# Optimization experiments

Measured on AMD Instinct MI355X. Metric: run time of the kernel, lower is better.

## Reference

```python
import jax, jax.numpy as jnp
import numpy as np

B, S, D, H = 2, 2048, 1024, 16
DH = D // H  # dim_per_head = 64


def setup_inputs() -> dict:
    key = jax.random.key(0)
    ks = jax.random.split(key, 12)
    scale = 1.0 / np.sqrt(D)
    inp = {
        "key": jax.random.normal(ks[0], (B, S, D), jnp.float32),
        "value": jax.random.normal(ks[1], (B, S, D), jnp.float32),
        "query": jax.random.normal(ks[2], (B, S, D), jnp.float32),
        "mask": jnp.zeros((B, S, S), dtype=bool),
        # nn.Linear weights stored as [out, in]; we keep [in, out] for x @ W
        "Wk": jax.random.normal(ks[3], (D, D), jnp.float32) * scale,
        "bk": jnp.zeros((D,), jnp.float32),
        "Wv": jax.random.normal(ks[4], (D, D), jnp.float32) * scale,
        "bv": jnp.zeros((D,), jnp.float32),
        "Wq": jax.random.normal(ks[5], (D, D), jnp.float32) * scale,
        "bq": jnp.zeros((D,), jnp.float32),
        "Wo": jax.random.normal(ks[6], (D, D), jnp.float32) * scale,
        "bo": jnp.zeros((D,), jnp.float32),
    }
    return inp


def reference(key, value, query, mask, Wk, bk, Wv, bv, Wq, bq, Wo, bo):
    # project and split heads: [B, S, D] -> [B, H, S, DH]
    def shape(x):
        return x.reshape(B, S, H, DH).transpose(0, 2, 1, 3)

    k = shape(key @ Wk + bk)
    v = shape(value @ Wv + bv)
    q = shape(query @ Wq + bq) / jnp.sqrt(jnp.asarray(DH, key.dtype))

    # scores: [B, H, Sq, Sk]
    scores = jnp.einsum("bhqd,bhkd->bhqk", q, k)
    scores = jnp.where(mask[:, None, :, :], jnp.asarray(-1e10, scores.dtype), scores)
    attn = jax.nn.softmax(scores, axis=-1)
    # dropout is identity in eval mode
    context = jnp.einsum("bhqk,bhkd->bhqd", attn, v)
    context = context.transpose(0, 2, 1, 3).reshape(B, S, D)
    output = context @ Wo + bo
    return output, attn
```

## Files before the change

### kernel.cpp

```cpp
#include <hip/hip_runtime.h>

#define B_  2
#define S_  2048
#define D_  1024
#define H_  16

typedef _Float16 h8 __attribute__((ext_vector_type(8)));
typedef _Float16 h4 __attribute__((ext_vector_type(4)));
typedef float f4 __attribute__((ext_vector_type(4)));

static __device__ __forceinline__ f4 mfma16(h8 a, h8 b, f4 c) {
  return __builtin_amdgcn_mfma_f32_16x16x32_f16(a, b, c, 0, 0, 0);
}

static __device__ __forceinline__ void gload16(const void* g, void* l) {
  __builtin_amdgcn_global_load_lds(
      (const __attribute__((address_space(1))) void*)g,
      (__attribute__((address_space(3))) void*)l, 16, 0, 0);
}

struct C3 { const float* in[3]; _Float16* out[3]; };
__global__ __launch_bounds__(256) void cvt3_kernel(C3 c) {
  const float* in = c.in[blockIdx.y];
  _Float16* out = c.out[blockIdx.y];
  const size_t i = ((size_t)blockIdx.x * 256 + threadIdx.x) * 8;
  float4 a = *(const float4*)(in + i);
  float4 b = *(const float4*)(in + i + 4);
  h8 v;
  v[0]=(_Float16)a.x; v[1]=(_Float16)a.y; v[2]=(_Float16)a.z; v[3]=(_Float16)a.w;
  v[4]=(_Float16)b.x; v[5]=(_Float16)b.y; v[6]=(_Float16)b.z; v[7]=(_Float16)b.w;
  *(h8*)(out + i) = v;
}

struct W4 { const float* w[4]; _Float16* wt[4]; };
__global__ __launch_bounds__(256) void wtrans4_kernel(W4 a) {
  const float* W = a.w[blockIdx.z];
  _Float16* WT = a.wt[blockIdx.z];
  __shared__ float tile[64][65];
  const int t = threadIdx.x;
  const int bi = blockIdx.x * 64;
  const int bj = blockIdx.y * 64;
  const int row = t >> 2, c0 = (t & 3) * 16;
  const float* src = W + (size_t)(bi + row) * D_ + bj + c0;
#pragma unroll
  for (int j = 0; j < 4; j++) {
    float4 v = *(const float4*)(src + j * 4);
    tile[row][c0 + j*4 + 0] = v.x; tile[row][c0 + j*4 + 1] = v.y;
    tile[row][c0 + j*4 + 2] = v.z; tile[row][c0 + j*4 + 3] = v.w;
  }
  __syncthreads();
  h8 o0, o1;
#pragma unroll
  for (int j = 0; j < 8; j++) o0[j] = (_Float16)tile[c0 + j][row];
#pragma unroll
  for (int j = 0; j < 8; j++) o1[j] = (_Float16)tile[c0 + 8 + j][row];
  _Float16* dst = WT + (size_t)(bj + row) * D_ + bi + c0;
  *(h8*)(dst)     = o0;
  *(h8*)(dst + 8) = o1;
}

__global__ __launch_bounds__(256) void maskflag_kernel(const unsigned char* __restrict__ mask,
                                                       unsigned char* __restrict__ flags) {
  __shared__ int s;
  const int t = threadIdx.x;
  const int kt = blockIdx.x, qb = blockIdx.y, b = blockIdx.z;
  if (t == 0) s = 0;
  __syncthreads();
  const unsigned char* mp = mask + ((size_t)(b * S_ + qb * 128 + (t >> 1))) * S_
                          + kt * 64 + (t & 1) * 32;
  const uint4* p = (const uint4*)mp;
  uint4 v = p[0], w = p[1];
  unsigned int o = v.x | v.y | v.z | v.w | w.x | w.y | w.z | w.w;
  if (o) s = 1;
  __syncthreads();
  if (t == 0) flags[((size_t)b * 16 + qb) * 32 + kt] = (unsigned char)s;
}

struct GArg { const _Float16* A; const _Float16* BT; const float* bias;
              void* out; float scale; int mode; };
struct G3 { GArg a[3]; };

__global__ __launch_bounds__(512, 4) void gemmz_kernel(G3 G) {
  const GArg g = G.a[blockIdx.z];
  const _Float16* __restrict__ A  = g.A;
  const _Float16* __restrict__ BT = g.BT;
  __shared__ _Float16 Ash[128 * 64];
  __shared__ _Float16 Bsh[128 * 64];
  const int t = threadIdx.x, lane = t & 63, wave = t >> 6;
  const int lrow = lane & 15, lq = lane >> 4;
  const int m0 = blockIdx.x * 128, n0 = blockIdx.y * 128;
  const int wm = wave >> 2, wn = wave & 3;
  f4 acc[4][2];
#pragma unroll
  for (int i = 0; i < 4; i++)
#pragma unroll
    for (int j = 0; j < 2; j++) acc[i][j] = f4{0.f, 0.f, 0.f, 0.f};
  float bb[2];
#pragma unroll
  for (int j = 0; j < 2; j++) bb[j] = g.bias[n0 + wn*32 + j*16 + lrow];

  const int srow = t >> 3;
  const int lch  = (t & 7) ^ (srow & 7);
  const _Float16* a0 = A  + (size_t)(m0 + srow)      * D_ + lch * 8;
  const _Float16* a1 = A  + (size_t)(m0 + 64 + srow) * D_ + lch * 8;
  const _Float16* b0 = BT + (size_t)(n0 + srow)      * D_ + lch * 8;
  const _Float16* b1 = BT + (size_t)(n0 + 64 + srow) * D_ + lch * 8;
  char* adst0 = (char*)Ash + wave * 1024;
  char* adst1 = (char*)Ash + 8192 + wave * 1024;
  char* bdst0 = (char*)Bsh + wave * 1024;
  char* bdst1 = (char*)Bsh + 8192 + wave * 1024;

  for (int k0 = 0; k0 < D_; k0 += 64) {
    gload16(a0 + k0, adst0);
    gload16(a1 + k0, adst1);
    gload16(b0 + k0, bdst0);
    gload16(b1 + k0, bdst1);
    __syncthreads();
#pragma unroll
    for (int kf = 0; kf < 2; kf++) {
      h8 af[4], bf[2];
#pragma unroll
      for (int i = 0; i < 4; i++) {
        int rr = wm*64 + i*16 + lrow;
        int ch = (kf*4 + lq) ^ (rr & 7);
        af[i] = *(h8*)((char*)Ash + rr*128 + ch*16);
      }
#pragma unroll
      for (int j = 0; j < 2; j++) {
        int rr = wn*32 + j*16 + lrow;
        int ch = (kf*4 + lq) ^ (rr & 7);
        bf[j] = *(h8*)((char*)Bsh + rr*128 + ch*16);
      }
#pragma unroll
      for (int i = 0; i < 4; i++)
#pragma unroll
        for (int j = 0; j < 2; j++)
          acc[i][j] = mfma16(af[i], bf[j], acc[i][j]);
    }
    __syncthreads();
  }

  if (g.mode == 0) {
    _Float16* out = (_Float16*)g.out;
#pragma unroll
    for (int i = 0; i < 4; i++) {
      int m = m0 + wm*64 + i*16 + lq*4;
#pragma unroll
      for (int j = 0; j < 2; j++) {
        int n = n0 + wn*32 + j*16 + lrow;
#pragma unroll
        for (int r = 0; r < 4; r++)
          out[(size_t)(m + r) * D_ + n] = (_Float16)((acc[i][j][r] + bb[j]) * g.scale);
      }
    }
  } else if (g.mode == 1) {
    _Float16* out = (_Float16*)g.out;
#pragma unroll
    for (int i = 0; i < 4; i++) {
      int m = m0 + wm*64 + i*16 + lq*4;
      int b = m >> 11, s = m & (S_ - 1);
#pragma unroll
      for (int j = 0; j < 2; j++) {
        int n = n0 + wn*32 + j*16 + lrow;
        int hh = n >> 6, dh = n & 63;
        h4 hv;
#pragma unroll
        for (int r = 0; r < 4; r++) hv[r] = (_Float16)(acc[i][j][r] + bb[j]);
        *(h4*)(out + ((size_t)((b * H_ + hh) * 64 + dh)) * S_ + s) = hv;
      }
    }
  } else {
    float* out = (float*)g.out;
#pragma unroll
    for (int i = 0; i < 4; i++) {
      int m = m0 + wm*64 + i*16 + lq*4;
#pragma unroll
      for (int j = 0; j < 2; j++) {
        int n = n0 + wn*32 + j*16 + lrow;
#pragma unroll
        for (int r = 0; r < 4; r++)
          out[(size_t)(m + r) * D_ + n] = acc[i][j][r] + bb[j];
      }
    }
  }
}


__global__ __launch_bounds__(256, 4) void attnA_kernel(
    const _Float16* __restrict__ Qp, const _Float16* __restrict__ Kp,
    const unsigned char* __restrict__ mask, const unsigned char* __restrict__ flags,
    float* __restrict__ Lbuf)
{
  __shared__ _Float16 Kt[256 * 64];
  const int t = threadIdx.x, lane = t & 63, wave = t >> 6;
  const int lrow = lane & 15, lq = lane >> 4;
  const int logical = ((blockIdx.x & 7) << 7) + (blockIdx.x >> 3);
  const int bh = logical >> 5, qb = logical & 31;
  const int b = bh >> 4, h = bh & 15;
  const int q0 = qb * 64, qw = q0 + wave * 16;

  h8 qf0, qf1;
  {
    const _Float16* qp = Qp + ((size_t)(b * S_ + qw + lrow)) * D_ + h * 64 + lq * 8;
    qf0 = *(const h8*)qp;
    qf1 = *(const h8*)(qp + 32);
  }

  const int srow = t >> 3, klch = (t & 7) ^ (srow & 7);
  const _Float16* ksrc = Kp + ((size_t)(b * S_ + srow)) * D_ + h * 64 + klch * 8;
  char* kdst = (char*)Kt + wave * 1024;
  const unsigned char* mflags = flags + ((size_t)(b * 16 + (qb >> 1))) * 32;

  float lsum[4] = {0.f, 0.f, 0.f, 0.f};
  for (int kt = 0; kt < S_; kt += 256) {
#pragma unroll
    for (int rnd = 0; rnd < 8; rnd++)
      gload16(ksrc + (size_t)(kt + rnd * 32) * D_, kdst + rnd * 4096);
    __syncthreads();
    const unsigned char* mrow = mask + ((size_t)(b * S_ + qw + lq*4)) * S_ + kt + lrow;
#pragma unroll
    for (int c = 0; c < 16; c++) {
      int kr = c*16 + lrow, sx = kr & 7;
      h8 k0 = *(h8*)((char*)Kt + kr*128 + ((lq     ^ sx) << 4));
      h8 k1 = *(h8*)((char*)Kt + kr*128 + (((4+lq) ^ sx) << 4));
      f4 a = f4{0.f, 0.f, 0.f, 0.f};
      a = mfma16(qf0, k0, a);
      a = mfma16(qf1, k1, a);
      if (mflags[(kt >> 6) + (c >> 2)]) {
#pragma unroll
        for (int r = 0; r < 4; r++)
          if (mrow[(size_t)r * S_ + c*16]) a[r] = -1e10f;
      }
#pragma unroll
      for (int r = 0; r < 4; r++) lsum[r] += __expf(fminf(a[r], 75.f));
    }
    __syncthreads();
  }

#pragma unroll
  for (int r = 0; r < 4; r++) {
    float cs = lsum[r];
#pragma unroll
    for (int d = 1; d < 16; d <<= 1) cs += __shfl_xor(cs, d);
    if (lrow == 0) Lbuf[((size_t)bh << 11) + qw + lq*4 + r] = 1.0f / cs;
  }
}

__global__ __launch_bounds__(256, 4) void attnB_kernel(
    const _Float16* __restrict__ Qp, const _Float16* __restrict__ Kp,
    const _Float16* __restrict__ VpT, const unsigned char* __restrict__ mask,
    const unsigned char* __restrict__ flags, const float* __restrict__ Lbuf,
    float* __restrict__ attn, _Float16* __restrict__ CtxH)
{
  __shared__ _Float16 Kt[128 * 64];
  __shared__ _Float16 Vt[64 * 128];
  __shared__ _Float16 Pt[64 * 64];
  const int t = threadIdx.x, lane = t & 63, wave = t >> 6;
  const int lrow = lane & 15, lq = lane >> 4;
  const int logical = ((blockIdx.x & 7) << 7) + (blockIdx.x >> 3);
  const int bh = logical >> 5, qb = logical & 31;
  const int b = bh >> 4, h = bh & 15;
  const int q0 = qb * 64, qw = q0 + wave * 16;

  h8 qf0, qf1;
  {
    const _Float16* qp = Qp + ((size_t)(b * S_ + qw + lrow)) * D_ + h * 64 + lq * 8;
    qf0 = *(const h8*)qp;
    qf1 = *(const h8*)(qp + 32);
  }
  float li[4];
#pragma unroll
  for (int r = 0; r < 4; r++) li[r] = Lbuf[((size_t)bh << 11) + qw + lq*4 + r];

  const int srow = t >> 3, klch = (t & 7) ^ (srow & 7);
  const _Float16* ksrc = Kp + ((size_t)(b * S_ + srow)) * D_ + h * 64 + klch * 8;
  char* kdst = (char*)Kt + wave * 1024;
  const int vrow = t >> 4, vlch = (t & 15) ^ (vrow & 15);
  const _Float16* vsrc = VpT + (size_t)bh * 64 * S_ + (size_t)vrow * S_ + vlch * 8;
  char* vdst = (char*)Vt + wave * 1024;
  const unsigned char* mflags = flags + ((size_t)(b * 16 + (qb >> 1))) * 32;

  f4 ctx[4];
#pragma unroll
  for (int dt = 0; dt < 4; dt++) ctx[dt] = f4{0.f, 0.f, 0.f, 0.f};

  for (int kt = 0; kt < S_; kt += 128) {
#pragma unroll
    for (int rnd = 0; rnd < 4; rnd++)
      gload16(ksrc + (size_t)(kt + rnd * 32) * D_, kdst + rnd * 4096);
#pragma unroll
    for (int rnd = 0; rnd < 4; rnd++)
      gload16(vsrc + (size_t)(rnd * 16) * S_ + kt, vdst + rnd * 4096);
    __syncthreads();

#pragma unroll
    for (int hh = 0; hh < 2; hh++) {
      const int kbase = kt + hh * 64;
      const bool mf = mflags[kbase >> 6] != 0;
      const unsigned char* mrow = mask + ((size_t)(b * S_ + qw + lq*4)) * S_ + kbase + lrow;
      const int prw = wave*16 + lq*4;
#pragma unroll
      for (int c = 0; c < 4; c++) {
        int kr = hh*64 + c*16 + lrow, sx = kr & 7;
        h8 k0 = *(h8*)((char*)Kt + kr*128 + ((lq     ^ sx) << 4));
        h8 k1 = *(h8*)((char*)Kt + kr*128 + (((4+lq) ^ sx) << 4));
        f4 a = f4{0.f, 0.f, 0.f, 0.f};
        a = mfma16(qf0, k0, a);
        a = mfma16(qf1, k1, a);
        if (mf) {
#pragma unroll
          for (int r = 0; r < 4; r++)
            if (mrow[(size_t)r * S_ + c*16]) a[r] = -1e10f;
        }
        float* ap = attn + ((size_t)bh * S_ + qw + lq*4) * S_ + kbase + c*16 + lrow;
        int eb = c*32 + lrow*2;
#pragma unroll
        for (int r = 0; r < 4; r++) {
          float p = __expf(fminf(a[r], 75.f)) * li[r];
          ap[(size_t)r * S_] = p;
          int rw = prw + r;
          *(_Float16*)((char*)Pt + rw*128 + ((((eb >> 4) ^ (rw & 7))) << 4) + (eb & 15))
              = (_Float16)p;
        }
      }
      {
        int pr2 = wave*16 + lrow, sxp = pr2 & 7;
        h8 pf0 = *(h8*)((char*)Pt + pr2*128 + (((    lq) ^ sxp) << 4));
        h8 pf1 = *(h8*)((char*)Pt + pr2*128 + (((4 + lq) ^ sxp) << 4));
#pragma unroll
        for (int dt = 0; dt < 4; dt++) {
          int vr = dt*16 + lrow, sxv = vr & 15;
          h8 vf0 = *(h8*)((char*)Vt + vr*256 + (((hh*8     + lq) ^ sxv) << 4));
          h8 vf1 = *(h8*)((char*)Vt + vr*256 + (((hh*8 + 4 + lq) ^ sxv) << 4));
          ctx[dt] = mfma16(pf0, vf0, ctx[dt]);
          ctx[dt] = mfma16(pf1, vf1, ctx[dt]);
        }
      }
    }
    __syncthreads();
  }

  _Float16* cp = CtxH + ((size_t)(b * S_ + qw + lq*4)) * D_ + h * 64 + lrow;
#pragma unroll
  for (int dt = 0; dt < 4; dt++)
#pragma unroll
    for (int r = 0; r < 4; r++)
      cp[(size_t)r * D_ + dt*16] = (_Float16)ctx[dt][r];
}

extern "C" void kernel_launch(void* const* d_in, const int* in_sizes, int n_in,
                              void* d_out, int out_size, void* d_ws, size_t ws_size,
                              hipStream_t stream) {
  const float* key   = (const float*)d_in[0];
  const float* value = (const float*)d_in[1];
  const float* query = (const float*)d_in[2];
  const unsigned char* mask = (const unsigned char*)d_in[3];
  const float* Wk = (const float*)d_in[4];
  const float* bk = (const float*)d_in[5];
  const float* Wv = (const float*)d_in[6];
  const float* bv = (const float*)d_in[7];
  const float* Wq = (const float*)d_in[8];
  const float* bq = (const float*)d_in[9];
  const float* Wo = (const float*)d_in[10];
  const float* bo = (const float*)d_in[11];

  char* ws = (char*)d_ws;
  _Float16* WkT  = (_Float16*)(ws + 0);
  _Float16* WvT  = (_Float16*)(ws + (size_t)2  * 1024 * 1024);
  _Float16* WqT  = (_Float16*)(ws + (size_t)4  * 1024 * 1024);
  _Float16* WoT  = (_Float16*)(ws + (size_t)6  * 1024 * 1024);
  _Float16* Qp   = (_Float16*)(ws + (size_t)8  * 1024 * 1024);
  _Float16* Kp   = (_Float16*)(ws + (size_t)16 * 1024 * 1024);
  _Float16* VpT  = (_Float16*)(ws + (size_t)24 * 1024 * 1024);
  _Float16* CtxH = (_Float16*)(ws + (size_t)32 * 1024 * 1024);
  unsigned char* flags = (unsigned char*)(ws + (size_t)40 * 1024 * 1024);
  float* Lbuf = (float*)(ws + (size_t)40 * 1024 * 1024 + 64 * 1024);

  float* outp = (float*)d_out;
  float* attn = outp + (size_t)B_ * S_ * D_;
  _Float16* qH = (_Float16*)(attn);
  _Float16* kH = (_Float16*)((char*)attn + (size_t)8  * 1024 * 1024);
  _Float16* vH = (_Float16*)((char*)attn + (size_t)16 * 1024 * 1024);

  C3 c{{query, key, value}, {qH, kH, vH}};
  cvt3_kernel<<<dim3(2048, 3), 256, 0, stream>>>(c);

  W4 w{{Wk, Wv, Wq, Wo}, {WkT, WvT, WqT, WoT}};
  wtrans4_kernel<<<dim3(16, 16, 4), 256, 0, stream>>>(w);

  maskflag_kernel<<<dim3(32, 16, 2), 256, 0, stream>>>(mask, flags);

  G3 gp{{{qH, WqT, bq, Qp, 0.125f, 0},
         {kH, WkT, bk, Kp, 1.0f,   0},
         {vH, WvT, bv, VpT, 1.0f,  1}}};
  gemmz_kernel<<<dim3(32, 8, 3), 512, 0, stream>>>(gp);

  attnA_kernel<<<1024, 256, 0, stream>>>(Qp, Kp, mask, flags, Lbuf);
  attnB_kernel<<<1024, 256, 0, stream>>>(Qp, Kp, VpT, mask, flags, Lbuf, attn, CtxH);

  G3 go{{{CtxH, WoT, bo, outp, 1.0f, 2},
         {nullptr, nullptr, nullptr, nullptr, 0.f, 2},
         {nullptr, nullptr, nullptr, nullptr, 0.f, 2}}};
  gemmz_kernel<<<dim3(32, 8, 1), 512, 0, stream>>>(go);
}
```

Measured before the change: 304.2 us.

## Double-buffer K/V tiles and process 128 query rows per attention block

Both attention kernels now give each wave 32 query rows instead of 16, so every K/V fragment read from shared memory feeds two MFMA groups. The grid is halved to 512 blocks. K and V tiles are double-buffered, so the next tile's global-to-LDS load is issued before the current tile is computed, which removes one barrier per iteration. The cost is twice the LDS and more registers, with occupancy hints cut from 4 to 2 blocks per CU.

Result: slower. 310.6 us (+2.1%).

```diff
diff --git a/kernel.cpp b/kernel.cpp
--- a/kernel.cpp
+++ b/kernel.cpp
@@ -186,166 +186,226 @@
 }
 
 
-__global__ __launch_bounds__(256, 4) void attnA_kernel(
+__global__ __launch_bounds__(256, 2) void attnA_kernel(
     const _Float16* __restrict__ Qp, const _Float16* __restrict__ Kp,
     const unsigned char* __restrict__ mask, const unsigned char* __restrict__ flags,
     float* __restrict__ Lbuf)
 {
-  __shared__ _Float16 Kt[256 * 64];
+  __shared__ _Float16 Kt[2 * 256 * 64];
   const int t = threadIdx.x, lane = t & 63, wave = t >> 6;
   const int lrow = lane & 15, lq = lane >> 4;
-  const int logical = ((blockIdx.x & 7) << 7) + (blockIdx.x >> 3);
-  const int bh = logical >> 5, qb = logical & 31;
+  const int logical = ((blockIdx.x & 7) << 6) + (blockIdx.x >> 3);
+  const int bh = logical >> 4, qb = logical & 15;
   const int b = bh >> 4, h = bh & 15;
-  const int q0 = qb * 64, qw = q0 + wave * 16;
-
-  h8 qf0, qf1;
-  {
-    const _Float16* qp = Qp + ((size_t)(b * S_ + qw + lrow)) * D_ + h * 64 + lq * 8;
-    qf0 = *(const h8*)qp;
-    qf1 = *(const h8*)(qp + 32);
+  const int q0 = qb * 128, qw = q0 + wave * 32;
+
+  h8 qf0[2], qf1[2];
+#pragma unroll
+  for (int g = 0; g < 2; g++) {
+    const _Float16* qp = Qp + ((size_t)(b * S_ + qw + g*16 + lrow)) * D_ + h * 64 + lq * 8;
+    qf0[g] = *(const h8*)qp;
+    qf1[g] = *(const h8*)(qp + 32);
   }
 
   const int srow = t >> 3, klch = (t & 7) ^ (srow & 7);
   const _Float16* ksrc = Kp + ((size_t)(b * S_ + srow)) * D_ + h * 64 + klch * 8;
-  char* kdst = (char*)Kt + wave * 1024;
-  const unsigned char* mflags = flags + ((size_t)(b * 16 + (qb >> 1))) * 32;
-
-  float lsum[4] = {0.f, 0.f, 0.f, 0.f};
+  const unsigned char* mflags = flags + ((size_t)(b * 16 + qb)) * 32;
+  const unsigned char* mrow0 = mask + ((size_t)(b * S_ + qw + lq*4)) * S_ + lrow;
+
+  float lsum[2][4];
+#pragma unroll
+  for (int g = 0; g < 2; g++)
+#pragma unroll
+    for (int r = 0; r < 4; r++) lsum[g][r] = 0.f;
+
+  {
+    char* kd = (char*)Kt + wave * 1024;
+#pragma unroll
+    for (int rnd = 0; rnd < 8; rnd++)
+      gload16(ksrc + (size_t)(rnd * 32) * D_, kd + rnd * 4096);
+  }
+  __syncthreads();
+  int cur = 0;
+
   for (int kt = 0; kt < S_; kt += 256) {
-#pragma unroll
-    for (int rnd = 0; rnd < 8; rnd++)
-      gload16(ksrc + (size_t)(kt + rnd * 32) * D_, kdst + rnd * 4096);
-    __syncthreads();
-    const unsigned char* mrow = mask + ((size_t)(b * S_ + qw + lq*4)) * S_ + kt + lrow;
+    if (kt + 256 < S_) {
+      char* kd = (char*)Kt + (cur ^ 1) * 32768 + wave * 1024;
+#pragma unroll
+      for (int rnd = 0; rnd < 8; rnd++)
+        gload16(ksrc + (size_t)(kt + 256 + rnd * 32) * D_, kd + rnd * 4096);
+    }
+    char* kb = (char*)Kt + cur * 32768;
 #pragma unroll
     for (int c = 0; c < 16; c++) {
       int kr = c*16 + lrow, sx = kr & 7;
-      h8 k0 = *(h8*)((char*)Kt + kr*128 + ((lq     ^ sx) << 4));
-      h8 k1 = *(h8*)((char*)Kt + kr*128 + (((4+lq) ^ sx) << 4));
-      f4 a = f4{0.f, 0.f, 0.f, 0.f};
-      a = mfma16(qf0, k0, a);
-      a = mfma16(qf1, k1, a);
-      if (mflags[(kt >> 6) + (c >> 2)]) {
-#pragma unroll
-        for (int r = 0; r < 4; r++)
-          if (mrow[(size_t)r * S_ + c*16]) a[r] = -1e10f;
-      }
-#pragma unroll
-      for (int r = 0; r < 4; r++) lsum[r] += __expf(fminf(a[r], 75.f));
+      h8 k0 = *(h8*)(kb + kr*128 + ((lq     ^ sx) << 4));
+      h8 k1 = *(h8*)(kb + kr*128 + (((4+lq) ^ sx) << 4));
+      const bool mf = mflags[(kt >> 6) + (c >> 2)] != 0;
+#pragma unroll
+      for (int g = 0; g < 2; g++) {
+        f4 a = f4{0.f, 0.f, 0.f, 0.f};
+        a = mfma16(qf0[g], k0, a);
+        a = mfma16(qf1[g], k1, a);
+        if (mf) {
+          const unsigned char* mr = mrow0 + (size_t)(g*16) * S_ + kt + c*16;
+#pragma unroll
+          for (int r = 0; r < 4; r++)
+            if (mr[(size_t)r * S_]) a[r] = -1e10f;
+        }
+#pragma unroll
+        for (int r = 0; r < 4; r++) lsum[g][r] += __expf(fminf(a[r], 75.f));
+      }
     }
     __syncthreads();
-  }
-
-#pragma unroll
-  for (int r = 0; r < 4; r++) {
-    float cs = lsum[r];
-#pragma unroll
-    for (int d = 1; d < 16; d <<= 1) cs += __shfl_xor(cs, d);
-    if (lrow == 0) Lbuf[((size_t)bh << 11) + qw + lq*4 + r] = 1.0f / cs;
-  }
-}
-
-__global__ __launch_bounds__(256, 4) void attnB_kernel(
+    cur ^= 1;
+  }
+
+#pragma unroll
+  for (int g = 0; g < 2; g++)
+#pragma unroll
+    for (int r = 0; r < 4; r++) {
+      float cs = lsum[g][r];
+#pragma unroll
+      for (int d = 1; d < 16; d <<= 1) cs += __shfl_xor(cs, d);
+      if (lrow == 0) Lbuf[((size_t)bh << 11) + qw + g*16 + lq*4 + r] = 1.0f / cs;
+    }
+}
+
+__global__ __launch_bounds__(256, 2) void attnB_kernel(
     const _Float16* __restrict__ Qp, const _Float16* __restrict__ Kp,
     const _Float16* __restrict__ VpT, const unsigned char* __restrict__ mask,
     const unsigned char* __restrict__ flags, const float* __restrict__ Lbuf,
     float* __restrict__ attn, _Float16* __restrict__ CtxH)
 {
-  __shared__ _Float16 Kt[128 * 64];
-  __shared__ _Float16 Vt[64 * 128];
-  __shared__ _Float16 Pt[64 * 64];
+  __shared__ _Float16 Kt[2 * 128 * 64];
+  __shared__ _Float16 Vt[2 * 64 * 128];
+  __shared__ _Float16 Pt[128 * 64];
   const int t = threadIdx.x, lane = t & 63, wave = t >> 6;
   const int lrow = lane & 15, lq = lane >> 4;
-  const int logical = ((blockIdx.x & 7) << 7) + (blockIdx.x >> 3);
-  const int bh = logical >> 5, qb = logical & 31;
+  const int logical = ((blockIdx.x & 7) << 6) + (blockIdx.x >> 3);
+  const int bh = logical >> 4, qb = logical & 15;
   const int b = bh >> 4, h = bh & 15;
-  const int q0 = qb * 64, qw = q0 + wave * 16;
-
-  h8 qf0, qf1;
-  {
-    const _Float16* qp = Qp + ((size_t)(b * S_ + qw + lrow)) * D_ + h * 64 + lq * 8;
-    qf0 = *(const h8*)qp;
-    qf1 = *(const h8*)(qp + 32);
-  }
-  float li[4];
-#pragma unroll
-  for (int r = 0; r < 4; r++) li[r] = Lbuf[((size_t)bh << 11) + qw + lq*4 + r];
+  const int q0 = qb * 128, qw = q0 + wave * 32;
+
+  h8 qf0[2], qf1[2];
+  float li[2][4];
+#pragma unroll
+  for (int g = 0; g < 2; g++) {
+    const _Float16* qp = Qp + ((size_t)(b * S_ + qw + g*16 + lrow)) * D_ + h * 64 + lq * 8;
+    qf0[g] = *(const h8*)qp;
+    qf1[g] = *(const h8*)(qp + 32);
+#pragma unroll
+    for (int r = 0; r < 4; r++)
+      li[g][r] = Lbuf[((size_t)bh << 11) + qw + g*16 + lq*4 + r];
+  }
 
   const int srow = t >> 3, klch = (t & 7) ^ (srow & 7);
   const _Float16* ksrc = Kp + ((size_t)(b * S_ + srow)) * D_ + h * 64 + klch * 8;
-  char* kdst = (char*)Kt + wave * 1024;
   const int vrow = t >> 4, vlch = (t & 15) ^ (vrow & 15);
   const _Float16* vsrc = VpT + (size_t)bh * 64 * S_ + (size_t)vrow * S_ + vlch * 8;
-  char* vdst = (char*)Vt + wave * 1024;
-  const unsigned char* mflags = flags + ((size_t)(b * 16 + (qb >> 1))) * 32;
-
-  f4 ctx[4];
-#pragma unroll
-  for (int dt = 0; dt < 4; dt++) ctx[dt] = f4{0.f, 0.f, 0.f, 0.f};
+  const unsigned char* mflags = flags + ((size_t)(b * 16 + qb)) * 32;
+  const unsigned char* mrow0 = mask + ((size_t)(b * S_ + qw + lq*4)) * S_ + lrow;
+
+  f4 ctx[2][4];
+#pragma unroll
+  for (int g = 0; g < 2; g++)
+#pragma unroll
+    for (int dt = 0; dt < 4; dt++) ctx[g][dt] = f4{0.f, 0.f, 0.f, 0.f};
+
+  {
+    char* kd = (char*)Kt + wave * 1024;
+    char* vd = (char*)Vt + wave * 1024;
+#pragma unroll
+    for (int rnd = 0; rnd < 4; rnd++)
+      gload16(ksrc + (size_t)(rnd * 32) * D_, kd + rnd * 4096);
+#pragma unroll
+    for (int rnd = 0; rnd < 4; rnd++)
+      gload16(vsrc + (size_t)(rnd * 16) * S_, vd + rnd * 4096);
+  }
+  __syncthreads();
+  int cur = 0;
 
   for (int kt = 0; kt < S_; kt += 128) {
-#pragma unroll
-    for (int rnd = 0; rnd < 4; rnd++)
-      gload16(ksrc + (size_t)(kt + rnd * 32) * D_, kdst + rnd * 4096);
-#pragma unroll
-    for (int rnd = 0; rnd < 4; rnd++)
-      gload16(vsrc + (size_t)(rnd * 16) * S_ + kt, vdst + rnd * 4096);
-    __syncthreads();
+    if (kt + 128 < S_) {
+      char* kd = (char*)Kt + (cur ^ 1) * 16384 + wave * 1024;
+      char* vd = (char*)Vt + (cur ^ 1) * 16384 + wave * 1024;
+#pragma unroll
+      for (int rnd = 0; rnd < 4; rnd++)
+        gload16(ksrc + (size_t)(kt + 128 + rnd * 32) * D_, kd + rnd * 4096);
+#pragma unroll
+      for (int rnd = 0; rnd < 4; rnd++)
+        gload16(vsrc + (size_t)(rnd * 16) * S_ + kt + 128, vd + rnd * 4096);
+    }
+    char* kb = (char*)Kt + cur * 16384;
+    char* vb = (char*)Vt + cur * 16384;
 
 #pragma unroll
     for (int hh = 0; hh < 2; hh++) {
       const int kbase = kt + hh * 64;
       const bool mf = mflags[kbase >> 6] != 0;
-      const unsigned char* mrow = mask + ((size_t)(b * S_ + qw + lq*4)) * S_ + kbase + lrow;
-      const int prw = wave*16 + lq*4;
 #pragma unroll
       for (int c = 0; c < 4; c++) {
         int kr = hh*64 + c*16 + lrow, sx = kr & 7;
-        h8 k0 = *(h8*)((char*)Kt + kr*128 + ((lq     ^ sx) << 4));
-        h8 k1 = *(h8*)((char*)Kt + kr*128 + (((4+lq) ^ sx) << 4));
-        f4 a = f4{0.f, 0.f, 0.f, 0.f};
-        a = mfma16(qf0, k0, a);
-        a = mfma16(qf1, k1, a);
-        if (mf) {
-#pragma unroll
-          for (int r = 0; r < 4; r++)
-            if (mrow[(size_t)r * S_ + c*16]) a[r] = -1e10f;
+        h8 k0 = *(h8*)(kb + kr*128 + ((lq     ^ sx) << 4));
+        h8 k1 = *(h8*)(kb + kr*128 + (((4+lq) ^ sx) << 4));
+        int eb = c*32 + lrow*2;
+#pragma unroll
+        for (int g = 0; g < 2; g++) {
+          f4 a = f4{0.f, 0.f, 0.f, 0.f};
+          a = mfma16(qf0[g], k0, a);
+          a = mfma16(qf1[g], k1, a);
+          if (mf) {
+            const unsigned char* mr = mrow0 + (size_t)(g*16) * S_ + kbase + c*16;
+#pragma unroll
+            for (int r = 0; r < 4; r++)
+              if (mr[(size_t)r * S_]) a[r] = -1e10f;
+          }
+          float* ap = attn + ((size_t)bh * S_ + qw + g*16 + lq*4) * S_ + kbase + c*16 + lrow;
+          const int rwb = wave*32 + g*16 + lq*4;
+#pragma unroll
+          for (int r = 0; r < 4; r++) {
+            float p = __expf(fminf(a[r], 75.f)) * li[g][r];
+            ap[(size_t)r * S_] = p;
+            int rw = rwb + r;
+            *(_Float16*)((char*)Pt + rw*128 + ((((eb >> 4) ^ (rw & 7))) << 4) + (eb & 15))
+                = (_Float16)p;
+          }
         }
-        float* ap = attn + ((size_t)bh * S_ + qw + lq*4) * S_ + kbase + c*16 + lrow;
-        int eb = c*32 + lrow*2;
-#pragma unroll
-        for (int r = 0; r < 4; r++) {
-          float p = __expf(fminf(a[r], 75.f)) * li[r];
-          ap[(size_t)r * S_] = p;
-          int rw = prw + r;
-          *(_Float16*)((char*)Pt + rw*128 + ((((eb >> 4) ^ (rw & 7))) << 4) + (eb & 15))
-              = (_Float16)p;
+      }
+      {
+        h8 pf0[2], pf1[2];
+#pragma unroll
+        for (int g = 0; g < 2; g++) {
+          int pr2 = wave*32 + g*16 + lrow, sxp = pr2 & 7;
+          pf0[g] = *(h8*)((char*)Pt + pr2*128 + (((    lq) ^ sxp) << 4));
+          pf1[g] = *(h8*)((char*)Pt + pr2*128 + (((4 + lq) ^ sxp) << 4));
         }
-      }
-      {
-        int pr2 = wave*16 + lrow, sxp = pr2 & 7;
-        h8 pf0 = *(h8*)((char*)Pt + pr2*128 + (((    lq) ^ sxp) << 4));
-        h8 pf1 = *(h8*)((char*)Pt + pr2*128 + (((4 + lq) ^ sxp) << 4));
 #pragma unroll
         for (int dt = 0; dt < 4; dt++) {
           int vr = dt*16 + lrow, sxv = vr & 15;
-          h8 vf0 = *(h8*)((char*)Vt + vr*256 + (((hh*8     + lq) ^ sxv) << 4));
-          h8 vf1 = *(h8*)((char*)Vt + vr*256 + (((hh*8 + 4 + lq) ^ sxv) << 4));
-          ctx[dt] = mfma16(pf0, vf0, ctx[dt]);
-          ctx[dt] = mfma16(pf1, vf1, ctx[dt]);
+          h8 vf0 = *(h8*)(vb + vr*256 + (((hh*8     + lq) ^ sxv) << 4));
+          h8 vf1 = *(h8*)(vb + vr*256 + (((hh*8 + 4 + lq) ^ sxv) << 4));
+#pragma unroll
+          for (int g = 0; g < 2; g++) {
+            ctx[g][dt] = mfma16(pf0[g], vf0, ctx[g][dt]);
+            ctx[g][dt] = mfma16(pf1[g], vf1, ctx[g][dt]);
+          }
         }
       }
     }
     __syncthreads();
-  }
-
-  _Float16* cp = CtxH + ((size_t)(b * S_ + qw + lq*4)) * D_ + h * 64 + lrow;
-#pragma unroll
-  for (int dt = 0; dt < 4; dt++)
-#pragma unroll
-    for (int r = 0; r < 4; r++)
-      cp[(size_t)r * D_ + dt*16] = (_Float16)ctx[dt][r];
+    cur ^= 1;
+  }
+
+#pragma unroll
+  for (int g = 0; g < 2; g++) {
+    _Float16* cp = CtxH + ((size_t)(b * S_ + qw + g*16 + lq*4)) * D_ + h * 64 + lrow;
+#pragma unroll
+    for (int dt = 0; dt < 4; dt++)
+#pragma unroll
+      for (int r = 0; r < 4; r++)
+        cp[(size_t)r * D_ + dt*16] = (_Float16)ctx[g][dt][r];
+  }
 }
 
 extern "C" void kernel_launch(void* const* d_in, const int* in_sizes, int n_in,
@@ -395,8 +455,8 @@
          {vH, WvT, bv, VpT, 1.0f,  1}}};
   gemmz_kernel<<<dim3(32, 8, 3), 512, 0, stream>>>(gp);
 
-  attnA_kernel<<<1024, 256, 0, stream>>>(Qp, Kp, mask, flags, Lbuf);
-  attnB_kernel<<<1024, 256, 0, stream>>>(Qp, Kp, VpT, mask, flags, Lbuf, attn, CtxH);
+  attnA_kernel<<<512, 256, 0, stream>>>(Qp, Kp, mask, flags, Lbuf);
+  attnB_kernel<<<512, 256, 0, stream>>>(Qp, Kp, VpT, mask, flags, Lbuf, attn, CtxH);
 
   G3 go{{{CtxH, WoT, bo, outp, 1.0f, 2},
          {nullptr, nullptr, nullptr, nullptr, 0.f, 2},
```
